# Kernel optimization log

Hardware: AMD Instinct MI355X
Metric: run time of the kernel (lower is better)

## Reference

```python
import jax, jax.numpy as jnp
import numpy as np

EPS = 1e-5

def conv2d(x, w, pad):
    # x: NCHW, w: OIHW, stride 1, symmetric padding
    return jax.lax.conv_general_dilated(
        x, w, window_strides=(1, 1), padding=[(pad, pad), (pad, pad)],
        dimension_numbers=('NCHW', 'OIHW', 'NCHW'))

def bn_eval(x, gamma, beta, mean, var):
    # eval-mode BatchNorm2d: per-channel affine with running stats
    s = gamma / jnp.sqrt(var + EPS)
    return x * s[None, :, None, None] + (beta - mean * s)[None, :, None, None]

def setup_inputs() -> dict:
    key = jax.random.key(0)
    ks = jax.random.split(key, 12)
    B, Cin, C, H, W = 2, 6, 64, 512, 512
    R, K = 4, 5                 # res_num, ksize
    Cf = 2 * 3 * K              # ch_out_final = 30
    d = {}
    d['feature_map'] = jax.random.normal(ks[0], (B, Cin, H, W), jnp.float32)
    d['base'] = jax.random.normal(ks[1], (B, 3, H, W), jnp.float32)
    d['w_first'] = jax.random.normal(ks[2], (C, Cin, 7, 7), jnp.float32) * 0.05
    d['kb_w1'] = jax.random.normal(ks[3], (R, C, C, 3, 3), jnp.float32) * 0.05
    d['kb_g1'] = jnp.ones((R, C), jnp.float32)
    d['kb_b1'] = jnp.zeros((R, C), jnp.float32)
    d['kb_m1'] = jax.random.normal(ks[4], (R, C), jnp.float32) * 0.1
    d['kb_v1'] = jax.random.uniform(ks[5], (R, C), jnp.float32) + 0.5
    d['kb_w2'] = jax.random.normal(ks[6], (R, C, C, 3, 3), jnp.float32) * 0.05
    d['kb_g2'] = jnp.ones((R, C), jnp.float32)
    d['kb_b2'] = jnp.zeros((R, C), jnp.float32)
    d['kb_m2'] = jax.random.normal(ks[7], (R, C), jnp.float32) * 0.1
    d['kb_v2'] = jax.random.uniform(ks[8], (R, C), jnp.float32) + 0.5
    d['w_last'] = jax.random.normal(ks[9], (Cf, C, 3, 3), jnp.float32) * 0.05
    return d

def reference(feature_map, base, w_first, kb_w1, kb_g1, kb_b1, kb_m1, kb_v1,
              kb_w2, kb_g2, kb_b2, kb_m2, kb_v2, w_last):
    K = 5
    P = K // 2
    b, _, h, w = base.shape
    # conv_first: 7x7 conv + ReLU
    y = jax.nn.relu(conv2d(feature_map, w_first, 3))
    # residual KB blocks: (conv3x3 -> BN -> ReLU) x2 + skip
    R = kb_w1.shape[0]
    for i in range(R):
        t = jax.nn.relu(bn_eval(conv2d(y, kb_w1[i], 1), kb_g1[i], kb_b1[i], kb_m1[i], kb_v1[i]))
        t = jax.nn.relu(bn_eval(conv2d(t, kb_w2[i], 1), kb_g2[i], kb_b2[i], kb_m2[i], kb_v2[i]))
        y = t + y
    # conv_last: [b, 2*3*K, h, w]
    y = conv2d(y, w_last, 1)
    Cf = y.shape[1]
    # [b,3,2K,h,w] -> [b,3,h,w,2K]
    weight = y.reshape(b, 3, Cf // 3, h, w).transpose(0, 1, 3, 4, 2)
    weight_h = jax.nn.softmax(weight[..., :K], axis=-1)  # [b,3,h,w,K]
    weight_w = jax.nn.softmax(weight[..., K:], axis=-1)
    # vertical adaptive filtering: pad H by P, unfold along H
    pad_h = jnp.pad(base, ((0, 0), (0, 0), (P, P), (0, 0)))
    unf_h = jnp.stack([pad_h[:, :, i:i + h, :] for i in range(K)], axis=-1)  # [b,3,h,w,K]
    filt_h = (unf_h * weight_h).sum(axis=-1)  # [b,3,h,w]
    # horizontal adaptive filtering: pad W by P, unfold along W
    pad_w = jnp.pad(filt_h, ((0, 0), (0, 0), (0, 0), (P, P)))
    unf_w = jnp.stack([pad_w[:, :, :, i:i + w] for i in range(K)], axis=-1)  # [b,3,h,w,K]
    return (unf_w * weight_w).sum(axis=-1)
```

## Files before the change

### kernel.cpp

```cpp
#include <hip/hip_runtime.h>
#include <math.h>

typedef __attribute__((ext_vector_type(8)))  short short8;
typedef __attribute__((ext_vector_type(4)))  float float4v;
typedef __attribute__((ext_vector_type(16))) float f32x16;
typedef unsigned int u32;

__device__ __forceinline__ unsigned short f2bf(float f) {
    union { float f; unsigned u; } x; x.f = f;
    unsigned r = x.u + 0x7FFFu + ((x.u >> 16) & 1u);
    return (unsigned short)(r >> 16);
}
__device__ __forceinline__ float bf2f(unsigned short u) {
    union { unsigned u; float f; } x; x.u = ((unsigned)u) << 16;
    return x.f;
}

__device__ __forceinline__ void gload16(const void* g, void* l) {
    __builtin_amdgcn_global_load_lds(
        (const __attribute__((address_space(1))) u32*)g,
        (__attribute__((address_space(3))) u32*)l, 16, 0, 0);
}

#define HWSZ ((size_t)512 * 512)

__global__ __launch_bounds__(256)
void prep7_k(const float* __restrict__ in, unsigned short* __restrict__ hi,
             unsigned short* __restrict__ lo)
{
    const int idx = blockIdx.x * 256 + threadIdx.x;
    const int b = idx >> 18, rem = idx & 262143;
    const int h = rem >> 9, w = rem & 511;
    unsigned short vh[8], vl[8];
#pragma unroll
    for (int c = 0; c < 8; ++c) {
        float x = (c < 6) ? in[((size_t)(b * 6 + c)) * HWSZ + (h << 9) + w] : 0.f;
        unsigned short h16 = f2bf(x);
        vh[c] = h16;
        vl[c] = f2bf(x - bf2f(h16));
    }
    const size_t o = ((size_t)idx) * 8;
    *(uint4*)(hi + o) = *(uint4*)vh;
    *(uint4*)(lo + o) = *(uint4*)vl;
}

__global__ __launch_bounds__(256)
void repack7_k(const float* __restrict__ wsrc, unsigned short* __restrict__ dhi,
               unsigned short* __restrict__ dlo)
{
    const int t = blockIdx.x * 256 + threadIdx.x;
    if (t >= 26624) return;
    const int j = t & 7, l = (t >> 3) & 63, ct = (t >> 9) & 3, kk = t >> 11;
    const int co = ct * 16 + (l & 15);
    const int s = kk * 4 + (l >> 4);
    float v = 0.f;
    if (s < 49 && j < 6)
        v = wsrc[((size_t)(co * 6 + j) * 7 + s / 7) * 7 + s % 7];
    unsigned short h16 = f2bf(v);
    dhi[t] = h16;
    dlo[t] = f2bf(v - bf2f(h16));
}

__global__ __launch_bounds__(256)
void conv7_mfma(const unsigned short* __restrict__ inhi,
                const unsigned short* __restrict__ inlo,
                const unsigned short* __restrict__ whi,
                const unsigned short* __restrict__ wlo,
                unsigned short* __restrict__ out)
{
    extern __shared__ char p_lds[];

    const int id = blockIdx.x;
    const int lid = (id & 7) * 256 + (id >> 3);
    const int w0 = (lid & 3) * 128;
    const int rest = lid >> 2;
    const int h0 = (rest & 255) * 2;
    const int b  = rest >> 8;

    const int tid = threadIdx.x;
    const int wv = tid >> 6, l = tid & 63, lq = l >> 4, lr = l & 15;

    for (int idx = tid; idx < 2144; idx += 256) {
        const int plane = idx >= 1072;
        const int rc = plane ? idx - 1072 : idx;
        const int r = rc / 134, c = rc % 134;
        const int hh = h0 - 3 + r, wc = w0 - 3 + c;
        int4 v = make_int4(0, 0, 0, 0);
        if (hh >= 0 && hh < 512 && wc >= 0 && wc < 512) {
            const unsigned short* src = plane ? inlo : inhi;
            v = *(const int4*)(src + ((((size_t)b * 512 + hh) * 512) + wc) * 8);
        }
        *(int4*)(p_lds + (size_t)idx * 16) = v;
    }
    __syncthreads();

    float4v acc[2][2][4];
#pragma unroll
    for (int pr = 0; pr < 2; ++pr)
#pragma unroll
        for (int pb = 0; pb < 2; ++pb)
#pragma unroll
            for (int ct = 0; ct < 4; ++ct)
                acc[pr][pb][ct] = (float4v){0.f, 0.f, 0.f, 0.f};

    const int cbase = wv * 32 + lr;
#pragma unroll
    for (int kk = 0; kk < 13; ++kk) {
        int s = kk * 4 + lq;
        if (s > 48) s = 48;
        const int dh = s / 7, dwd = s % 7;
        short8 ah[2][2], al[2][2];
#pragma unroll
        for (int pr = 0; pr < 2; ++pr)
#pragma unroll
            for (int pb = 0; pb < 2; ++pb) {
                const int off = ((pr + dh) * 134 + cbase + pb * 16 + dwd) * 16;
                ah[pr][pb] = *(const short8*)(p_lds + off);
                al[pr][pb] = *(const short8*)(p_lds + 17152 + off);
            }
#pragma unroll
        for (int ct = 0; ct < 4; ++ct) {
            const short8 bh = *(const short8*)(whi + ((size_t)(kk * 4 + ct) * 64 + l) * 8);
            const short8 bl = *(const short8*)(wlo + ((size_t)(kk * 4 + ct) * 64 + l) * 8);
#pragma unroll
            for (int pr = 0; pr < 2; ++pr)
#pragma unroll
                for (int pb = 0; pb < 2; ++pb) {
                    acc[pr][pb][ct] = __builtin_amdgcn_mfma_f32_16x16x32_bf16(ah[pr][pb], bh, acc[pr][pb][ct], 0, 0, 0);
                    acc[pr][pb][ct] = __builtin_amdgcn_mfma_f32_16x16x32_bf16(al[pr][pb], bh, acc[pr][pb][ct], 0, 0, 0);
                    acc[pr][pb][ct] = __builtin_amdgcn_mfma_f32_16x16x32_bf16(ah[pr][pb], bl, acc[pr][pb][ct], 0, 0, 0);
                }
        }
    }

#pragma unroll
    for (int pr = 0; pr < 2; ++pr) {
        const int h = h0 + pr;
#pragma unroll
        for (int pb = 0; pb < 2; ++pb) {
            const int col0 = w0 + wv * 32 + pb * 16 + lq * 4;
#pragma unroll
            for (int ct = 0; ct < 4; ++ct) {
                const int half = ct >> 1, colocal = (ct & 1) * 16 + lr;
#pragma unroll
                for (int rg = 0; rg < 4; ++rg) {
                    const size_t o = ((((size_t)(b * 2 + half) * 512 + h) * 512) + (col0 + rg)) * 32 + colocal;
                    out[o] = f2bf(fmaxf(acc[pr][pb][ct][rg], 0.f));
                }
            }
        }
    }
}

__global__ __launch_bounds__(256)
void repack3n_k(const float* __restrict__ w1, const float* __restrict__ w2,
                const float* __restrict__ g1, const float* __restrict__ v1,
                const float* __restrict__ g2, const float* __restrict__ v2,
                unsigned short* __restrict__ dst)
{
    const int conv = blockIdx.z;
    const float* src = (conv < 4) ? (w1 + (size_t)conv * 36864) : (w2 + (size_t)(conv - 4) * 36864);
    const float* g = (conv < 4) ? (g1 + conv * 64) : (g2 + (conv - 4) * 64);
    const float* vv = (conv < 4) ? (v1 + conv * 64) : (v2 + (conv - 4) * 64);
    unsigned short* d = dst + (size_t)conv * 36864;

    const int t = blockIdx.x * 256 + threadIdx.x;
    const int j = t & 7, l = (t >> 3) & 63;
    const int rest = t >> 9;
    const int s = rest % 9, m = rest / 9;
    const int ch = m & 1, q = m >> 1;
    const int co = ch * 32 + (l & 31);
    const int ci = q * 16 + (l >> 5) * 8 + j;
    const float sc = g[co] * rsqrtf(vv[co] + 1e-5f);
    d[t] = f2bf(src[((size_t)co * 64 + ci) * 9 + s] * sc);
}

__global__ __launch_bounds__(256)
void bias8_k(const float* __restrict__ g1, const float* __restrict__ b1,
             const float* __restrict__ m1, const float* __restrict__ v1,
             const float* __restrict__ g2, const float* __restrict__ b2,
             const float* __restrict__ m2, const float* __restrict__ v2,
             float* __restrict__ bias)
{
    const int t = blockIdx.x * 256 + threadIdx.x;
    if (t >= 512) return;
    const int conv = t >> 6, co = t & 63;
    const float* g = (conv < 4) ? (g1 + conv * 64) : (g2 + (conv - 4) * 64);
    const float* be = (conv < 4) ? (b1 + conv * 64) : (b2 + (conv - 4) * 64);
    const float* mn = (conv < 4) ? (m1 + conv * 64) : (m2 + (conv - 4) * 64);
    const float* vv = (conv < 4) ? (v1 + conv * 64) : (v2 + (conv - 4) * 64);
    const float sc = g[co] * rsqrtf(vv[co] + 1e-5f);
    bias[t] = be[co] - mn[co] * sc;
}

template <bool ADD_>
__global__ __launch_bounds__(512)
void conv3_mfma32(const unsigned short* __restrict__ in,
                  const unsigned short* __restrict__ wrp,
                  const float* __restrict__ bias,
                  const unsigned short* __restrict__ skip,
                  unsigned short* __restrict__ out)
{
    extern __shared__ char smem[];
    char* w_lds = smem;
    char* p_lds = smem + 18432;

    const int id = blockIdx.x;
    const int lid = (id & 7) * 128 + (id >> 3);
    const int w0 = (lid & 3) * 128;
    const int h0 = ((lid >> 2) & 127) * 4;
    const int b  = lid >> 9;

    const int tid = threadIdx.x;
    const int wv = tid >> 6, l = tid & 63;
    const int rw = wv >> 1, tq = wv & 1;
    const int lo5 = l & 31, hi = l >> 5;

    f32x16 acc[2][2];
#pragma unroll
    for (int ch = 0; ch < 2; ++ch)
#pragma unroll
        for (int t4 = 0; t4 < 2; ++t4)
#pragma unroll
            for (int e = 0; e < 16; ++e) acc[ch][t4][e] = 0.f;

    for (int q = 0; q < 4; ++q) {
        if (q) __syncthreads();

        const unsigned short* wq  = wrp + (size_t)q * 9216;
        const unsigned short* inp = in + (size_t)(b * 2 + (q >> 1)) * HWSZ * 32;
        const int cb8 = (q & 1) * 2;

        for (int i = wv; i < 42; i += 8) {
            if (i < 18) {
                gload16(wq + (size_t)i * 512 + l * 8, w_lds + (size_t)i * 1024);
            } else {
                const int j2 = i - 18, p = j2 >> 1, half = j2 & 1;
                const int row = p >> 1, kg = p & 1;
                const int hh = h0 - 1 + row;
                if (hh >= 0 && hh < 512)
                    gload16(inp + ((size_t)hh * 512 + w0 + half * 64 + l) * 32 + (cb8 + kg) * 8,
                            p_lds + (size_t)(p * 132 + 1 + half * 64) * 16);
            }
        }
        if (tid < 24) {
            const int p = tid >> 1, side = tid & 1;
            const int row = p >> 1, kg = p & 1;
            const int hh = h0 - 1 + row;
            const int wc = side ? (w0 + 128) : (w0 - 1);
            int4 v = make_int4(0, 0, 0, 0);
            if (hh >= 0 && hh < 512 && wc >= 0 && wc < 512)
                v = *(const int4*)(inp + ((size_t)hh * 512 + wc) * 32 + (cb8 + kg) * 8);
            *(int4*)(p_lds + (size_t)(p * 132 + (side ? 129 : 0)) * 16) = v;
        }
        if (h0 == 0) {
            for (int g = tid; g < 264; g += 512)
                *(int4*)(p_lds + (size_t)g * 16) = make_int4(0, 0, 0, 0);
        } else if (h0 == 508) {
            for (int g = tid; g < 264; g += 512)
                *(int4*)(p_lds + (size_t)(10 * 132 + g) * 16) = make_int4(0, 0, 0, 0);
        }
        __syncthreads();

#pragma unroll
        for (int s = 0; s < 9; ++s) {
            const int dh = s / 3, dwd = s % 3;
            const int row = rw + dh;
            short8 pf[2];
#pragma unroll
            for (int t4 = 0; t4 < 2; ++t4) {
                const int px = tq * 64 + t4 * 32 + dwd + lo5;
                pf[t4] = *(const short8*)(p_lds +
                    ((size_t)((row * 2 + hi) * 132 + px)) * 16);
            }
#pragma unroll
            for (int ch = 0; ch < 2; ++ch) {
                const short8 w8 = *(const short8*)(w_lds +
                    ((size_t)((ch * 9 + s) * 64 + l)) * 16);
#pragma unroll
                for (int t4 = 0; t4 < 2; ++t4)
                    acc[ch][t4] = __builtin_amdgcn_mfma_f32_32x32x16_bf16(
                        pf[t4], w8, acc[ch][t4], 0, 0, 0);
            }
        }
    }

    const int h = h0 + rw;
#pragma unroll
    for (int ch = 0; ch < 2; ++ch) {
        const float bvs = bias[ch * 32 + lo5];
        const size_t pbase = ((size_t)(b * 2 + ch) * HWSZ + (size_t)h * 512);
#pragma unroll
        for (int t4 = 0; t4 < 2; ++t4) {
#pragma unroll
            for (int reg = 0; reg < 16; ++reg) {
                const int pxl = tq * 64 + t4 * 32 + (reg & 3) + 8 * (reg >> 2) + 4 * hi;
                const size_t o = (pbase + (w0 + pxl)) * 32 + lo5;
                float v = fmaxf(acc[ch][t4][reg] + bvs, 0.f);
                if (ADD_) v += bf2f(skip[o]);
                out[o] = f2bf(v);
            }
        }
    }
}

__global__ __launch_bounds__(256)
void repackLn_k(const float* __restrict__ wsrc, unsigned short* __restrict__ d)
{
    const int t = blockIdx.x * 256 + threadIdx.x;
    const int j = t & 7, l = (t >> 3) & 63;
    const int rest = t >> 9;
    const int s = rest % 9, q = rest / 9;
    const int co = l & 31;
    const int ci = q * 16 + (l >> 5) * 8 + j;
    d[t] = (co < 30) ? f2bf(wsrc[((size_t)co * 64 + ci) * 9 + s]) : (unsigned short)0;
}

__global__ __launch_bounds__(256)
void conv_lastN(const unsigned short* __restrict__ in,
                const unsigned short* __restrict__ wrp,
                unsigned short* __restrict__ out)
{
    extern __shared__ char smem[];
    char* w_lds = smem;
    char* p_lds = smem + 36864;

    const int id = blockIdx.x;
    const int lid = (id & 7) * 256 + (id >> 3);
    const int w0 = (lid & 3) * 128;
    const int h0 = ((lid >> 2) & 255) * 2;
    const int b  = lid >> 10;

    const int tid = threadIdx.x;
    const int wv = tid >> 6, l = tid & 63;
    const int rw = wv >> 1, tq = wv & 1;
    const int lo5 = l & 31, hi = l >> 5;

    f32x16 acc[2];
#pragma unroll
    for (int t4 = 0; t4 < 2; ++t4)
#pragma unroll
        for (int e = 0; e < 16; ++e) acc[t4][e] = 0.f;

    for (int q = 0; q < 4; ++q) {
        if (q) __syncthreads();

        const unsigned short* inp = in + (size_t)(b * 2 + (q >> 1)) * HWSZ * 32;
        const int cb8 = (q & 1) * 2;

        if (q == 0)
            for (int i = wv; i < 36; i += 4)
                gload16(wrp + (size_t)i * 512 + l * 8, w_lds + (size_t)i * 1024);
        for (int i = wv; i < 16; i += 4) {
            const int p = i >> 1, half = i & 1;
            const int row = p >> 1, kg = p & 1;
            const int hh = h0 - 1 + row;
            if (hh >= 0 && hh < 512)
                gload16(inp + ((size_t)hh * 512 + w0 + half * 64 + l) * 32 + (cb8 + kg) * 8,
                        p_lds + (size_t)(p * 132 + 1 + half * 64) * 16);
        }
        if (tid < 16) {
            const int p = tid >> 1, side = tid & 1;
            const int row = p >> 1, kg = p & 1;
            const int hh = h0 - 1 + row;
            const int wc = side ? (w0 + 128) : (w0 - 1);
            int4 v = make_int4(0, 0, 0, 0);
            if (hh >= 0 && hh < 512 && wc >= 0 && wc < 512)
                v = *(const int4*)(inp + ((size_t)hh * 512 + wc) * 32 + (cb8 + kg) * 8);
            *(int4*)(p_lds + (size_t)(p * 132 + (side ? 129 : 0)) * 16) = v;
        }
        if (h0 == 0) {
            for (int g = tid; g < 264; g += 256)
                *(int4*)(p_lds + (size_t)g * 16) = make_int4(0, 0, 0, 0);
        } else if (h0 == 510) {
            for (int g = tid; g < 264; g += 256)
                *(int4*)(p_lds + (size_t)(6 * 132 + g) * 16) = make_int4(0, 0, 0, 0);
        }
        __syncthreads();

#pragma unroll
        for (int s = 0; s < 9; ++s) {
            const int dh = s / 3, dwd = s % 3;
            const int row = rw + dh;
            const short8 wf = *(const short8*)(w_lds + ((size_t)((q * 9 + s) * 64 + l)) * 16);
#pragma unroll
            for (int t4 = 0; t4 < 2; ++t4) {
                const int px = tq * 64 + t4 * 32 + dwd + lo5;
                const short8 pf = *(const short8*)(p_lds +
                    ((size_t)((row * 2 + hi) * 132 + px)) * 16);
                acc[t4] = __builtin_amdgcn_mfma_f32_32x32x16_bf16(wf, pf, acc[t4], 0, 0, 0);
            }
        }
    }

    const int h = h0 + rw;
#pragma unroll
    for (int t4 = 0; t4 < 2; ++t4) {
        const int px = w0 + tq * 64 + t4 * 32 + lo5;
#pragma unroll
        for (int reg = 0; reg < 16; ++reg) {
            const int co = (reg & 3) + 8 * (reg >> 2) + 4 * hi;
            if (co < 30)
                out[(((size_t)(b * 30 + co) * 512 + h) * 512) + px] = f2bf(acc[t4][reg]);
        }
    }
}

__global__ __launch_bounds__(256)
void filt_fused_k(const unsigned short* __restrict__ wl, const float* __restrict__ base,
                  float* __restrict__ out)
{
    __shared__ float F[516];

    const int id = blockIdx.x;
    const int lid = (id & 7) * 384 + (id >> 3);
    const int h = lid & 511;
    const int bc = lid >> 9;
    const int b = bc / 3, c = bc % 3;
    const int t = threadIdx.x;

    if (t < 2) F[t] = 0.f;
    if (t >= 254) F[t + 260] = 0.f;

    const size_t rowoff = (size_t)h * 512;
    const unsigned short* wv_p = wl + ((size_t)(b * 30 + c * 10) * HWSZ) + rowoff;
    const unsigned short* wh_p = wv_p + 5 * HWSZ;
    const float* bp = base + (size_t)bc * HWSZ;

#pragma unroll
    for (int wi = 0; wi < 2; ++wi) {
        const int w = t + wi * 256;
        float v[5]; float mx = -1e30f;
#pragma unroll
        for (int i = 0; i < 5; ++i) { v[i] = bf2f(wv_p[(size_t)i * HWSZ + w]); mx = fmaxf(mx, v[i]); }
        float sm = 0.f;
#pragma unroll
        for (int i = 0; i < 5; ++i) { v[i] = __expf(v[i] - mx); sm += v[i]; }
        const float inv = 1.f / sm;
        float acc = 0.f;
#pragma unroll
        for (int i = 0; i < 5; ++i) {
            const int hh = h + i - 2;
            const float bvv = (hh >= 0 && hh < 512) ? bp[(size_t)hh * 512 + w] : 0.f;
            acc = fmaf(bvv, v[i] * inv, acc);
        }
        F[w + 2] = acc;
    }
    __syncthreads();

#pragma unroll
    for (int wi = 0; wi < 2; ++wi) {
        const int w = t + wi * 256;
        float v[5]; float mx = -1e30f;
#pragma unroll
        for (int i = 0; i < 5; ++i) { v[i] = bf2f(wh_p[(size_t)i * HWSZ + w]); mx = fmaxf(mx, v[i]); }
        float sm = 0.f;
#pragma unroll
        for (int i = 0; i < 5; ++i) { v[i] = __expf(v[i] - mx); sm += v[i]; }
        const float inv = 1.f / sm;
        float acc = 0.f;
#pragma unroll
        for (int i = 0; i < 5; ++i)
            acc = fmaf(F[w + i], v[i] * inv, acc);
        out[(size_t)bc * HWSZ + rowoff + w] = acc;
    }
}

extern "C" void kernel_launch(void* const* d_in, const int* in_sizes, int n_in,
                              void* d_out, int out_size, void* d_ws, size_t ws_size,
                              hipStream_t stream)
{
    const float* fm      = (const float*)d_in[0];
    const float* base    = (const float*)d_in[1];
    const float* w_first = (const float*)d_in[2];
    const float* kb_w1   = (const float*)d_in[3];
    const float* kb_g1   = (const float*)d_in[4];
    const float* kb_b1   = (const float*)d_in[5];
    const float* kb_m1   = (const float*)d_in[6];
    const float* kb_v1   = (const float*)d_in[7];
    const float* kb_w2   = (const float*)d_in[8];
    const float* kb_g2   = (const float*)d_in[9];
    const float* kb_b2   = (const float*)d_in[10];
    const float* kb_m2   = (const float*)d_in[11];
    const float* kb_v2   = (const float*)d_in[12];
    const float* w_last  = (const float*)d_in[13];

    char* ws = (char*)d_ws;
    unsigned short* wrp3n  = (unsigned short*)ws;
    unsigned short* wrpL   = wrp3n + (size_t)8 * 36864;
    unsigned short* wrp7hi = wrpL + 18432;
    unsigned short* wrp7lo = wrp7hi + 26624;
    float*          biasws = (float*)(wrp7lo + 26624);
    unsigned short* actA = (unsigned short*)(ws + (1 << 20));
    unsigned short* actB = actA + (size_t)2 * HWSZ * 64;
    unsigned short* actC = actB + (size_t)2 * HWSZ * 64;
    unsigned short* in7hi = actB;
    unsigned short* in7lo = actB + (size_t)2 * HWSZ * 8;
    unsigned short* logits = actC;

    hipFuncSetAttribute((const void*)conv3_mfma32<false>,
                        hipFuncAttributeMaxDynamicSharedMemorySize, 43776);
    hipFuncSetAttribute((const void*)conv3_mfma32<true>,
                        hipFuncAttributeMaxDynamicSharedMemorySize, 43776);
    hipFuncSetAttribute((const void*)conv_lastN,
                        hipFuncAttributeMaxDynamicSharedMemorySize, 53760);
    hipFuncSetAttribute((const void*)conv7_mfma,
                        hipFuncAttributeMaxDynamicSharedMemorySize, 34304);

    dim3 blk(256);

    repack3n_k<<<dim3(144, 1, 8), blk, 0, stream>>>(kb_w1, kb_w2, kb_g1, kb_v1, kb_g2, kb_v2, wrp3n);
    bias8_k<<<dim3(2, 1, 1), blk, 0, stream>>>(kb_g1, kb_b1, kb_m1, kb_v1, kb_g2, kb_b2, kb_m2, kb_v2, biasws);
    repackLn_k<<<dim3(72, 1, 1), blk, 0, stream>>>(w_last, wrpL);
    repack7_k<<<dim3(104, 1, 1), blk, 0, stream>>>(w_first, wrp7hi, wrp7lo);
    prep7_k<<<dim3(2048, 1, 1), blk, 0, stream>>>(fm, in7hi, in7lo);

    conv7_mfma<<<dim3(2048, 1, 1), blk, 34304, stream>>>(in7hi, in7lo, wrp7hi, wrp7lo, actA);

    unsigned short* cur = actA;
    unsigned short* oth = actC;
    for (int i = 0; i < 4; ++i) {
        conv3_mfma32<false><<<dim3(1024, 1, 1), dim3(512), 43776, stream>>>(
            cur, wrp3n + (size_t)i * 36864, biasws + i * 64, nullptr, actB);
        conv3_mfma32<true><<<dim3(1024, 1, 1), dim3(512), 43776, stream>>>(
            actB, wrp3n + (size_t)(4 + i) * 36864, biasws + (4 + i) * 64, cur, oth);
        unsigned short* t = cur; cur = oth; oth = t;
    }

    conv_lastN<<<dim3(2048, 1, 1), blk, 53760, stream>>>(cur, wrpL, logits);

    filt_fused_k<<<dim3(3072, 1, 1), blk, 0, stream>>>(logits, base, (float*)d_out);
}
```

Measured before the change: 540.9 us.

## Double-buffer input patches and preload all weights in conv3 and conv_last

The 3x3 residual conv kernel now loads all four channel-quarter weight slices into LDS up front and double-buffers the input patch. The next quarter's patch is fetched while MFMAs run on the current one, and one barrier per quarter replaces the two used before. conv_last gets the same double-buffering. The cost is much larger LDS use (about 124KB per 512-thread block for conv3), which cuts blocks per CU to one and can reduce latency hiding across blocks.

```diff
diff --git a/kernel.cpp b/kernel.cpp
--- a/kernel.cpp
+++ b/kernel.cpp
@@ -203,7 +203,8 @@
 {
     extern __shared__ char smem[];
     char* w_lds = smem;
-    char* p_lds = smem + 18432;
+    char* pbuf0 = smem + 73728;
+    char* pbuf1 = pbuf0 + 25344;
 
     const int id = blockIdx.x;
     const int lid = (id & 7) * 128 + (id >> 3);
@@ -216,32 +217,16 @@
     const int rw = wv >> 1, tq = wv & 1;
     const int lo5 = l & 31, hi = l >> 5;
 
-    f32x16 acc[2][2];
-#pragma unroll
-    for (int ch = 0; ch < 2; ++ch)
-#pragma unroll
-        for (int t4 = 0; t4 < 2; ++t4)
-#pragma unroll
-            for (int e = 0; e < 16; ++e) acc[ch][t4][e] = 0.f;
-
-    for (int q = 0; q < 4; ++q) {
-        if (q) __syncthreads();
-
-        const unsigned short* wq  = wrp + (size_t)q * 9216;
+    auto stage_patch = [&](char* pl, int q) {
         const unsigned short* inp = in + (size_t)(b * 2 + (q >> 1)) * HWSZ * 32;
         const int cb8 = (q & 1) * 2;
-
-        for (int i = wv; i < 42; i += 8) {
-            if (i < 18) {
-                gload16(wq + (size_t)i * 512 + l * 8, w_lds + (size_t)i * 1024);
-            } else {
-                const int j2 = i - 18, p = j2 >> 1, half = j2 & 1;
-                const int row = p >> 1, kg = p & 1;
-                const int hh = h0 - 1 + row;
-                if (hh >= 0 && hh < 512)
-                    gload16(inp + ((size_t)hh * 512 + w0 + half * 64 + l) * 32 + (cb8 + kg) * 8,
-                            p_lds + (size_t)(p * 132 + 1 + half * 64) * 16);
-            }
+        for (int i = wv; i < 24; i += 8) {
+            const int p = i >> 1, half = i & 1;
+            const int row = p >> 1, kg = p & 1;
+            const int hh = h0 - 1 + row;
+            if (hh >= 0 && hh < 512)
+                gload16(inp + ((size_t)hh * 512 + w0 + half * 64 + l) * 32 + (cb8 + kg) * 8,
+                        pl + (size_t)(p * 132 + 1 + half * 64) * 16);
         }
         if (tid < 24) {
             const int p = tid >> 1, side = tid & 1;
@@ -251,16 +236,34 @@
             int4 v = make_int4(0, 0, 0, 0);
             if (hh >= 0 && hh < 512 && wc >= 0 && wc < 512)
                 v = *(const int4*)(inp + ((size_t)hh * 512 + wc) * 32 + (cb8 + kg) * 8);
-            *(int4*)(p_lds + (size_t)(p * 132 + (side ? 129 : 0)) * 16) = v;
+            *(int4*)(pl + (size_t)(p * 132 + (side ? 129 : 0)) * 16) = v;
         }
         if (h0 == 0) {
             for (int g = tid; g < 264; g += 512)
-                *(int4*)(p_lds + (size_t)g * 16) = make_int4(0, 0, 0, 0);
+                *(int4*)(pl + (size_t)g * 16) = make_int4(0, 0, 0, 0);
         } else if (h0 == 508) {
             for (int g = tid; g < 264; g += 512)
-                *(int4*)(p_lds + (size_t)(10 * 132 + g) * 16) = make_int4(0, 0, 0, 0);
-        }
-        __syncthreads();
+                *(int4*)(pl + (size_t)(10 * 132 + g) * 16) = make_int4(0, 0, 0, 0);
+        }
+    };
+
+    f32x16 acc[2][2];
+#pragma unroll
+    for (int ch = 0; ch < 2; ++ch)
+#pragma unroll
+        for (int t4 = 0; t4 < 2; ++t4)
+#pragma unroll
+            for (int e = 0; e < 16; ++e) acc[ch][t4][e] = 0.f;
+
+    for (int i = wv; i < 72; i += 8)
+        gload16(wrp + (size_t)i * 512 + l * 8, w_lds + (size_t)i * 1024);
+    stage_patch(pbuf0, 0);
+    __syncthreads();
+
+    for (int q = 0; q < 4; ++q) {
+        char* cur = (q & 1) ? pbuf1 : pbuf0;
+        char* nxt = (q & 1) ? pbuf0 : pbuf1;
+        if (q < 3) stage_patch(nxt, q + 1);
 
 #pragma unroll
         for (int s = 0; s < 9; ++s) {
@@ -270,19 +273,20 @@
 #pragma unroll
             for (int t4 = 0; t4 < 2; ++t4) {
                 const int px = tq * 64 + t4 * 32 + dwd + lo5;
-                pf[t4] = *(const short8*)(p_lds +
+                pf[t4] = *(const short8*)(cur +
                     ((size_t)((row * 2 + hi) * 132 + px)) * 16);
             }
 #pragma unroll
             for (int ch = 0; ch < 2; ++ch) {
                 const short8 w8 = *(const short8*)(w_lds +
-                    ((size_t)((ch * 9 + s) * 64 + l)) * 16);
+                    ((size_t)q * 18432) + ((size_t)((ch * 9 + s) * 64 + l)) * 16);
 #pragma unroll
                 for (int t4 = 0; t4 < 2; ++t4)
                     acc[ch][t4] = __builtin_amdgcn_mfma_f32_32x32x16_bf16(
                         pf[t4], w8, acc[ch][t4], 0, 0, 0);
             }
         }
+        __syncthreads();
     }
 
     const int h = h0 + rw;
@@ -323,7 +327,8 @@
 {
     extern __shared__ char smem[];
     char* w_lds = smem;
-    char* p_lds = smem + 36864;
+    char* pbuf0 = smem + 36864;
+    char* pbuf1 = pbuf0 + 16896;
 
     const int id = blockIdx.x;
     const int lid = (id & 7) * 256 + (id >> 3);
@@ -336,28 +341,16 @@
     const int rw = wv >> 1, tq = wv & 1;
     const int lo5 = l & 31, hi = l >> 5;
 
-    f32x16 acc[2];
-#pragma unroll
-    for (int t4 = 0; t4 < 2; ++t4)
-#pragma unroll
-        for (int e = 0; e < 16; ++e) acc[t4][e] = 0.f;
-
-    for (int q = 0; q < 4; ++q) {
-        if (q) __syncthreads();
-
+    auto stage_patch = [&](char* pl, int q) {
         const unsigned short* inp = in + (size_t)(b * 2 + (q >> 1)) * HWSZ * 32;
         const int cb8 = (q & 1) * 2;
-
-        if (q == 0)
-            for (int i = wv; i < 36; i += 4)
-                gload16(wrp + (size_t)i * 512 + l * 8, w_lds + (size_t)i * 1024);
         for (int i = wv; i < 16; i += 4) {
             const int p = i >> 1, half = i & 1;
             const int row = p >> 1, kg = p & 1;
             const int hh = h0 - 1 + row;
             if (hh >= 0 && hh < 512)
                 gload16(inp + ((size_t)hh * 512 + w0 + half * 64 + l) * 32 + (cb8 + kg) * 8,
-                        p_lds + (size_t)(p * 132 + 1 + half * 64) * 16);
+                        pl + (size_t)(p * 132 + 1 + half * 64) * 16);
         }
         if (tid < 16) {
             const int p = tid >> 1, side = tid & 1;
@@ -367,16 +360,32 @@
             int4 v = make_int4(0, 0, 0, 0);
             if (hh >= 0 && hh < 512 && wc >= 0 && wc < 512)
                 v = *(const int4*)(inp + ((size_t)hh * 512 + wc) * 32 + (cb8 + kg) * 8);
-            *(int4*)(p_lds + (size_t)(p * 132 + (side ? 129 : 0)) * 16) = v;
+            *(int4*)(pl + (size_t)(p * 132 + (side ? 129 : 0)) * 16) = v;
         }
         if (h0 == 0) {
             for (int g = tid; g < 264; g += 256)
-                *(int4*)(p_lds + (size_t)g * 16) = make_int4(0, 0, 0, 0);
+                *(int4*)(pl + (size_t)g * 16) = make_int4(0, 0, 0, 0);
         } else if (h0 == 510) {
             for (int g = tid; g < 264; g += 256)
-                *(int4*)(p_lds + (size_t)(6 * 132 + g) * 16) = make_int4(0, 0, 0, 0);
-        }
-        __syncthreads();
+                *(int4*)(pl + (size_t)(6 * 132 + g) * 16) = make_int4(0, 0, 0, 0);
+        }
+    };
+
+    f32x16 acc[2];
+#pragma unroll
+    for (int t4 = 0; t4 < 2; ++t4)
+#pragma unroll
+        for (int e = 0; e < 16; ++e) acc[t4][e] = 0.f;
+
+    for (int i = wv; i < 36; i += 4)
+        gload16(wrp + (size_t)i * 512 + l * 8, w_lds + (size_t)i * 1024);
+    stage_patch(pbuf0, 0);
+    __syncthreads();
+
+    for (int q = 0; q < 4; ++q) {
+        char* cur = (q & 1) ? pbuf1 : pbuf0;
+        char* nxt = (q & 1) ? pbuf0 : pbuf1;
+        if (q < 3) stage_patch(nxt, q + 1);
 
 #pragma unroll
         for (int s = 0; s < 9; ++s) {
@@ -386,11 +395,12 @@
 #pragma unroll
             for (int t4 = 0; t4 < 2; ++t4) {
                 const int px = tq * 64 + t4 * 32 + dwd + lo5;
-                const short8 pf = *(const short8*)(p_lds +
+                const short8 pf = *(const short8*)(cur +
                     ((size_t)((row * 2 + hi) * 132 + px)) * 16);
                 acc[t4] = __builtin_amdgcn_mfma_f32_32x32x16_bf16(wf, pf, acc[t4], 0, 0, 0);
             }
         }
+        __syncthreads();
     }
 
     const int h = h0 + rw;
@@ -499,11 +509,11 @@
     unsigned short* logits = actC;
 
     hipFuncSetAttribute((const void*)conv3_mfma32<false>,
-                        hipFuncAttributeMaxDynamicSharedMemorySize, 43776);
+                        hipFuncAttributeMaxDynamicSharedMemorySize, 124416);
     hipFuncSetAttribute((const void*)conv3_mfma32<true>,
-                        hipFuncAttributeMaxDynamicSharedMemorySize, 43776);
+                        hipFuncAttributeMaxDynamicSharedMemorySize, 124416);
     hipFuncSetAttribute((const void*)conv_lastN,
-                        hipFuncAttributeMaxDynamicSharedMemorySize, 53760);
+                        hipFuncAttributeMaxDynamicSharedMemorySize, 70656);
     hipFuncSetAttribute((const void*)conv7_mfma,
                         hipFuncAttributeMaxDynamicSharedMemorySize, 34304);
 
@@ -520,14 +530,14 @@
     unsigned short* cur = actA;
     unsigned short* oth = actC;
     for (int i = 0; i < 4; ++i) {
-        conv3_mfma32<false><<<dim3(1024, 1, 1), dim3(512), 43776, stream>>>(
+        conv3_mfma32<false><<<dim3(1024, 1, 1), dim3(512), 124416, stream>>>(
             cur, wrp3n + (size_t)i * 36864, biasws + i * 64, nullptr, actB);
-        conv3_mfma32<true><<<dim3(1024, 1, 1), dim3(512), 43776, stream>>>(
+        conv3_mfma32<true><<<dim3(1024, 1, 1), dim3(512), 124416, stream>>>(
             actB, wrp3n + (size_t)(4 + i) * 36864, biasws + (4 + i) * 64, cur, oth);
         unsigned short* t = cur; cur = oth; oth = t;
     }
 
-    conv_lastN<<<dim3(2048, 1, 1), blk, 53760, stream>>>(cur, wrpL, logits);
+    conv_lastN<<<dim3(2048, 1, 1), blk, 70656, stream>>>(cur, wrpL, logits);
 
     filt_fused_k<<<dim3(3072, 1, 1), blk, 0, stream>>>(logits, base, (float*)d_out);
 }
```

Measured after the change: 590.6 us. 9.2% more time.
